# Optimization experiments

Measured on AMD Instinct MI355X. Metric: run time of the kernel, lower is better.

The kernel has to match this reference:

```python
import jax, jax.numpy as jnp
import numpy as np

B, N_SIDE, S = 64, 40, 512
N = N_SIDE * N_SIDE          # 1600 grid points (fl_feature_dims [1,40,40])
EMB = 10                     # embedding_dim
GDIM = 8                     # lie('homography').dim
WIDTH = 128
C1 = 20                      # first-layer output channels


def _embed(x, emb_dim):
    # sinusoidal embedding of each scalar coordinate: [..., D] -> [..., D*emb_dim]
    freqs = 2.0 ** jnp.arange(emb_dim // 2, dtype=x.dtype)
    ang = x[..., None] * freqs                       # [..., D, emb/2]
    e = jnp.concatenate([jnp.sin(ang), jnp.cos(ang)], axis=-1)  # [..., D, emb]
    return e.reshape(x.shape[:-1] + (x.shape[-1] * emb_dim,))


def _glorot(key, shape):
    fan_in = shape[0]
    return jax.random.normal(key, shape, dtype=jnp.float32) / np.sqrt(fan_in)


def setup_inputs() -> dict:
    key = jax.random.key(0)
    ks = jax.random.split(key, 16)
    inp = {
        'data':   jax.random.normal(ks[0], (B, N, 1), dtype=jnp.float32),
        'v0':     jax.random.normal(ks[1], (S, GDIM), dtype=jnp.float32),
        'v_last': jax.random.normal(ks[2], (S, GDIM), dtype=jnp.float32),
        # FirstLayer filter MLP: 2*EMB -> 20 -> 20 -> 1*C1
        'fl_w1': _glorot(ks[3], (2 * EMB, 20)), 'fl_b1': jnp.zeros((20,), jnp.float32),
        'fl_w2': _glorot(ks[4], (20, 20)),      'fl_b2': jnp.zeros((20,), jnp.float32),
        'fl_w3': _glorot(ks[5], (20, C1)),      'fl_b3': jnp.zeros((C1,), jnp.float32),
        # Hidden FilterMLP: EMB*GDIM=80 -> WIDTH -> C1*WIDTH
        's_w1': _glorot(ks[6], (EMB * GDIM, WIDTH)), 's_b1': jnp.zeros((WIDTH,), jnp.float32),
        's_w2': _glorot(ks[7], (WIDTH, C1 * WIDTH)), 's_b2': jnp.zeros((C1 * WIDTH,), jnp.float32),
        'fc1_w': _glorot(ks[8], (WIDTH, WIDTH)), 'fc1_b': jnp.zeros((WIDTH,), jnp.float32),
        'fc2_w': _glorot(ks[9], (WIDTH, WIDTH)), 'fc2_b': jnp.zeros((WIDTH,), jnp.float32),
        'pool_w': _glorot(ks[10], (WIDTH, 10)),  'pool_b': jnp.zeros((10,), jnp.float32),
    }
    return inp


def reference(data, v0, v_last, fl_w1, fl_b1, fl_w2, fl_b2, fl_w3, fl_b3,
              s_w1, s_b1, s_w2, s_b2, fc1_w, fc1_b, fc2_w, fc2_b, pool_w, pool_b):
    silu = jax.nn.silu
    # pixel grid in [-1,1]^2, homogeneous coords [N,3]
    lin = jnp.linspace(-1.0, 1.0, N_SIDE, dtype=data.dtype)
    xx, yy = jnp.meshgrid(lin, lin, indexing='ij')
    coords = jnp.stack([xx.ravel(), yy.ravel()], axis=-1)           # [N,2]
    xh = jnp.concatenate([coords, jnp.ones((N, 1), data.dtype)], -1)  # [N,3]
    # homography matrices: identity + small perturbation from 8 group params
    pert = jnp.concatenate([0.1 * v_last, jnp.zeros((S, 1), data.dtype)], -1).reshape(S, 3, 3)
    H = jnp.eye(3, dtype=data.dtype) + pert                          # [S,3,3]
    y = jnp.einsum('sij,nj->sni', H, xh)                             # [S,N,3]
    t = y[..., :2] / y[..., 2:3]                                     # projective action [S,N,2]
    # continuous-kernel first layer: filters generated by MLP on embedded coords
    e1 = _embed(t, EMB)                                              # [S,N,20]
    h = silu(e1 @ fl_w1 + fl_b1)
    h = silu(h @ fl_w2 + fl_b2)
    filt1 = h @ fl_w3 + fl_b3                                        # [S,N,C1]
    z = jnp.einsum('bn,sno->bso', data[:, :, 0], filt1) / N          # [B,S,C1]
    z = silu(z)
    # hidden FilterMLP on group samples v0 -> per-sample filters [S,C1,WIDTH]
    v0e = _embed(v0, EMB)                                            # [S,80]
    h2 = silu(v0e @ s_w1 + s_b1)                                     # [S,WIDTH]
    filt2 = (h2 @ s_w2 + s_b2).reshape(S, C1, WIDTH)
    # (1/S) * sum over group-sample and channel axes of broadcast product
    z = jnp.einsum('bsc,scw->bw', z, filt2) / S                      # [B,WIDTH]
    z = silu(z @ fc1_w + fc1_b) + z
    z = silu(z @ fc2_w + fc2_b) + z
    return z @ pool_w + pool_b                                       # [B,10]
```

## Files before the change

kernel.cpp:

```cpp
#include <hip/hip_runtime.h>

#define N_PTS 1600
#define NSIDE 40
#define SNUM  512
#define BNUM  64
#define C1D   20
#define WID   128

typedef _Float16 h8  __attribute__((ext_vector_type(8)));
typedef _Float16 h4  __attribute__((ext_vector_type(4)));
typedef __fp16   h2v __attribute__((ext_vector_type(2)));
typedef float    f4  __attribute__((ext_vector_type(4)));

__device__ __forceinline__ float silu_f(float x){ return x / (1.f + __expf(-x)); }
__device__ __forceinline__ void fma4(float4& a, float s, const float4 w){
    a.x += s*w.x; a.y += s*w.y; a.z += s*w.z; a.w += s*w.w;
}

__global__ __launch_bounds__(256) void ka_prep(
    const float* __restrict__ data, const float* __restrict__ v0,
    const float* __restrict__ s_w1, const float* __restrict__ s_b1,
    const float* __restrict__ s_w2, const float* __restrict__ s_b2,
    const float* __restrict__ w1, const float* __restrict__ b1,
    const float* __restrict__ w2, const float* __restrict__ b2,
    const float* __restrict__ w3, const float* __restrict__ b3,
    _Float16* __restrict__ dataA, float* __restrict__ f2g,
    _Float16* __restrict__ wPackA, float* __restrict__ bPackA,
    float* __restrict__ out2g)
{
    const int t  = threadIdx.x;
    const int bx = blockIdx.x;
    if (bx == 370) {
        const float* wsrc[3] = { w1, w2, w3 };
        const float* bsrc[3] = { b1, b2, b3 };
        for (int v = t; v < 3072; v += 256) {
            const int l = v >> 10, rem = v & 1023;
            const int cout = rem >> 5, cin = rem & 31;
            float x = 0.f;
            if (cout < 20 && cin < 20) x = wsrc[l][cin * 20 + cout];
            wPackA[v] = (_Float16)x;
        }
        if (t < 96) {
            const int l = t >> 5, cout = t & 31;
            bPackA[t] = (cout < 20) ? bsrc[l][cout] : 0.f;
        }
        for (int v = t; v < 8192; v += 256) out2g[v] = 0.f;
        return;
    }
    if (bx >= 320) {
        const int o  = (bx - 320) * 256 + t;
        const int L  = o & 63, cm = o >> 6;
        const int mt = cm & 3, ch = cm >> 2;
        const int b  = mt * 16 + (L & 15);
        const int nb = ch * 32 + (L >> 4) * 8;
        const float* src = data + b * N_PTS + nb;
        h8 v;
        #pragma unroll
        for (int j = 0; j < 8; j++) v[j] = (_Float16)src[j];
        *(h8*)(dataA + (size_t)o * 8) = v;
        return;
    }
    const int st  = bx / 10, ct = bx - st * 10;
    const int s0  = st * 16;
    const int col = ct * 256 + t;
    __shared__ __align__(16) float h2t[128][20];

    for (int idx = t; idx < 2048; idx += 256) {
        const int ss = idx >> 7, j = idx & 127;
        float acc = s_b1[j];
        #pragma unroll
        for (int d = 0; d < 8; d++) {
            const float val = v0[(s0 + ss) * 8 + d];
            float sv, cv;
            __sincosf(val, &sv, &cv);
            #pragma unroll
            for (int k = 0; k < 5; k++) {
                acc += sv * s_w1[(d*10 + k)     * WID + j];
                acc += cv * s_w1[(d*10 + 5 + k) * WID + j];
                const float ns = 2.f * sv * cv;
                const float nc = 1.f - 2.f * sv * sv;
                sv = ns; cv = nc;
            }
        }
        h2t[j][ss] = silu_f(acc);
    }
    __syncthreads();

    float4 acc[4];
    #pragma unroll
    for (int qq = 0; qq < 4; qq++) acc[qq] = make_float4(0.f, 0.f, 0.f, 0.f);
    #pragma unroll 4
    for (int i = 0; i < 128; i++) {
        const float wv = s_w2[i * 2560 + col];
        const float4* hh = (const float4*)&h2t[i][0];
        #pragma unroll
        for (int qq = 0; qq < 4; qq++) fma4(acc[qq], wv, hh[qq]);
    }
    const float bias = s_b2[col];
    const float* af = (const float*)acc;
    #pragma unroll
    for (int ss = 0; ss < 16; ss++)
        f2g[(s0 + ss) * 2560 + col] = af[ss] + bias;
}

__device__ __forceinline__ void embed_pt(int n, const float Hm[9], h2v e2[10])
{
    const int i = n / NSIDE;
    const int j = n - i * NSIDE;
    const float x = -1.f + (float)i * (2.f/39.f);
    const float y = -1.f + (float)j * (2.f/39.f);
    const float y0 = Hm[0]*x + Hm[1]*y + Hm[2];
    const float y1 = Hm[3]*x + Hm[4]*y + Hm[5];
    const float y2 = Hm[6]*x + Hm[7]*y + Hm[8];
    const float inv = 1.f / y2;
    const float t0 = y0 * inv, t1 = y1 * inv;
    float e[20];
    float sv0, cv0, sv1, cv1;
    __sincosf(t0, &sv0, &cv0);
    __sincosf(t1, &sv1, &cv1);
    #pragma unroll
    for (int k = 0; k < 5; k++) {
        e[k] = sv0; e[5+k] = cv0; e[10+k] = sv1; e[15+k] = cv1;
        const float ns0 = 2.f*sv0*cv0, nc0 = 1.f - 2.f*sv0*sv0; sv0 = ns0; cv0 = nc0;
        const float ns1 = 2.f*sv1*cv1, nc1 = 1.f - 2.f*sv1*sv1; sv1 = ns1; cv1 = nc1;
    }
    #pragma unroll
    for (int k = 0; k < 10; k++)
        e2[k] = __builtin_amdgcn_cvt_pkrtz(e[2*k], e[2*k+1]);
}

#define ASTRIDE 40

__global__ __launch_bounds__(256) void k1_filt_z(
    const _Float16* __restrict__ dataA, const float* __restrict__ v_last,
    const _Float16* __restrict__ wPackA, const float* __restrict__ bPackA,
    float* __restrict__ zpart)
{
    const int s    = blockIdx.x & 511;
    const int half = blockIdx.x >> 9;
    const int nb0  = half * 800;
    const int t    = threadIdx.x;
    const int lane = t & 63;
    const int w    = t >> 6;
    const int q    = lane >> 4;
    const int l15  = lane & 15;

    __shared__ __align__(16) unsigned char pool[21504];
    __shared__ __align__(16) _Float16 filtB[20 * 264];
    _Float16* act = (_Float16*)pool;
    float*    red = (float*)pool;

    h8 wf[3][2]; float bv[3][2];
    #pragma unroll
    for (int l = 0; l < 3; l++)
        #pragma unroll
        for (int nt = 0; nt < 2; nt++) {
            wf[l][nt] = *(const h8*)(wPackA + (((l*2+nt)*16 + l15) * 32 + q*8));
            bv[l][nt] = bPackA[(l*2+nt)*16 + l15];
        }

    float Hm[9];
    #pragma unroll
    for (int k = 0; k < 9; k++) Hm[k] = (k == 0 || k == 4 || k == 8) ? 1.f : 0.f;
    #pragma unroll
    for (int k = 0; k < 8; k++) Hm[k] += 0.1f * v_last[s*8 + k];

    f4 zacc[4][2];
    #pragma unroll
    for (int mt = 0; mt < 4; mt++) { zacc[mt][0] = (f4)(0.f); zacc[mt][1] = (f4)(0.f); }
    const f4 zero4 = (f4)(0.f);

    {
        unsigned long long* pz = (unsigned long long*)(act + t*ASTRIDE + 20);
        pz[0] = 0ull; pz[1] = 0ull; pz[2] = 0ull;
    }

    for (int base = 0; base < 800; base += 256) {
        const int tn = min(256, 800 - base);
        if (t < tn) {
            h2v e2[10];
            embed_pt(nb0 + base + t, Hm, e2);
            #pragma unroll
            for (int k = 0; k < 10; k++)
                *(h2v*)(act + t*ASTRIDE + 2*k) = e2[k];
        }
        __syncthreads();

        const int nmt = tn >> 4;
        #pragma unroll
        for (int l = 0; l < 3; l++) {
            for (int mt = w; mt < nmt; mt += 4) {
                const int r0 = mt * 16;
                const h8 af = *(const h8*)(act + (r0 + l15)*ASTRIDE + q*8);
                f4 D0 = __builtin_amdgcn_mfma_f32_16x16x32_f16(af, wf[l][0], zero4, 0, 0, 0);
                f4 D1 = __builtin_amdgcn_mfma_f32_16x16x32_f16(af, wf[l][1], zero4, 0, 0, 0);
                if (l < 2) {
                    #pragma unroll
                    for (int r = 0; r < 4; r++) {
                        const int p = r0 + q*4 + r;
                        act[p*ASTRIDE + l15] = (_Float16)silu_f(D0[r] + bv[l][0]);
                        if (l15 < 4)
                            act[p*ASTRIDE + 16 + l15] = (_Float16)silu_f(D1[r] + bv[l][1]);
                    }
                } else {
                    h4 p0, p1;
                    #pragma unroll
                    for (int r = 0; r < 4; r++) {
                        p0[r] = (_Float16)(D0[r] + bv[2][0]);
                        p1[r] = (_Float16)(D1[r] + bv[2][1]);
                    }
                    *(h4*)(filtB + l15*264 + r0 + q*4) = p0;
                    if (l15 < 4)
                        *(h4*)(filtB + (16 + l15)*264 + r0 + q*4) = p1;
                }
            }
        }
        __syncthreads();

        const int nkc = tn >> 5;
        const int r1row = (l15 < 4) ? (16 + l15) : 0;
        for (int kc = w; kc < nkc; kc += 4) {
            const int gchunk = ((nb0 + base) >> 5) + kc;
            const h8 bf0 = *(const h8*)(filtB + l15  *264 + kc*32 + q*8);
            const h8 bf1 = *(const h8*)(filtB + r1row*264 + kc*32 + q*8);
            #pragma unroll
            for (int mt = 0; mt < 4; mt++) {
                const h8 afz = *(const h8*)(dataA + ((size_t)(gchunk*4 + mt)*64 + lane)*8);
                zacc[mt][0] = __builtin_amdgcn_mfma_f32_16x16x32_f16(afz, bf0, zacc[mt][0], 0, 0, 0);
                zacc[mt][1] = __builtin_amdgcn_mfma_f32_16x16x32_f16(afz, bf1, zacc[mt][1], 0, 0, 0);
            }
        }
        __syncthreads();
    }

    #pragma unroll
    for (int mt = 0; mt < 4; mt++) {
        #pragma unroll
        for (int r = 0; r < 4; r++) {
            const int b = mt*16 + q*4 + r;
            red[(w*64 + b)*21 + l15] = zacc[mt][0][r];
            if (l15 < 4) red[(w*64 + b)*21 + 16 + l15] = zacc[mt][1][r];
        }
    }
    __syncthreads();
    for (int v = t; v < 1280; v += 256) {
        const int c = v >> 6, b = v & 63;
        const float sum = red[b*21 + c] + red[(64+b)*21 + c]
                        + red[(128+b)*21 + c] + red[(192+b)*21 + c];
        zpart[(half*512 + s)*1280 + v] = sum;
    }
}

__global__ __launch_bounds__(256) void k2_contract(
    const float* __restrict__ zg, const float* __restrict__ f2g,
    float* __restrict__ out2g)
{
    const int blk = blockIdx.x;
    const int sg  = blk >> 1;
    const int wh  = blk & 1;
    const int s0  = sg * 4;
    const int w0  = wh * 64;
    const int t   = threadIdx.x;
    __shared__ __align__(16) float zl[4*1280];
    __shared__ __align__(16) float fl[4*20*64];
    #pragma unroll
    for (int sp = 0; sp < 4; sp++) {
        const int srow = (s0 + sp) * 1280;
        for (int r = t; r < 1280; r += 256) {
            const float a0 = zg[srow + r];
            const float a1 = zg[512*1280 + srow + r];
            zl[sp*1280 + r] = silu_f((a0 + a1) * (1.f / (float)N_PTS));
        }
        for (int u = t; u < 1280; u += 256) {
            const int c = u >> 6, ww = u & 63;
            fl[sp*1280 + u] = f2g[(s0 + sp)*2560 + c*128 + w0 + ww];
        }
    }
    __syncthreads();
    const int ww = t & 63, bh = t >> 6;
    float4 acc[4];
    #pragma unroll
    for (int qq = 0; qq < 4; qq++) acc[qq] = make_float4(0.f, 0.f, 0.f, 0.f);
    #pragma unroll 4
    for (int sc = 0; sc < 80; sc++) {
        const float f = fl[sc * 64 + ww];
        const float4* zz = (const float4*)&zl[sc * 64 + bh * 16];
        #pragma unroll
        for (int qq = 0; qq < 4; qq++) fma4(acc[qq], f, zz[qq]);
    }
    const float* af = (const float*)acc;
    #pragma unroll
    for (int idx = 0; idx < 16; idx++) {
        const int b = bh * 16 + idx;
        atomicAdd(&out2g[b * 128 + w0 + ww], af[idx]);
    }
}

__global__ __launch_bounds__(128) void k3_tail(
    const float* __restrict__ out2g,
    const float* __restrict__ fc1w, const float* __restrict__ fc1b,
    const float* __restrict__ fc2w, const float* __restrict__ fc2b,
    const float* __restrict__ pw,   const float* __restrict__ pb,
    float* __restrict__ out)
{
    const int b = blockIdx.x, t = threadIdx.x;
    __shared__ float zb[128], r1[128], r2[128];
    zb[t] = out2g[b * 128 + t] * (1.f / (float)SNUM);
    __syncthreads();
    float a = fc1b[t];
    #pragma unroll 8
    for (int i = 0; i < 128; i++) a += zb[i] * fc1w[i * 128 + t];
    r1[t] = silu_f(a) + zb[t];
    __syncthreads();
    a = fc2b[t];
    #pragma unroll 8
    for (int i = 0; i < 128; i++) a += r1[i] * fc2w[i * 128 + t];
    r2[t] = silu_f(a) + r1[t];
    __syncthreads();
    if (t < 10) {
        float o = pb[t];
        #pragma unroll 8
        for (int i = 0; i < 128; i++) o += r2[i] * pw[i * 10 + t];
        out[b * 10 + t] = o;
    }
}

extern "C" void kernel_launch(void* const* d_in, const int* in_sizes, int n_in,
                              void* d_out, int out_size, void* d_ws, size_t ws_size,
                              hipStream_t stream) {
    const float* data   = (const float*)d_in[0];
    const float* v0     = (const float*)d_in[1];
    const float* v_last = (const float*)d_in[2];
    const float* fl_w1  = (const float*)d_in[3];
    const float* fl_b1  = (const float*)d_in[4];
    const float* fl_w2  = (const float*)d_in[5];
    const float* fl_b2  = (const float*)d_in[6];
    const float* fl_w3  = (const float*)d_in[7];
    const float* fl_b3  = (const float*)d_in[8];
    const float* s_w1   = (const float*)d_in[9];
    const float* s_b1   = (const float*)d_in[10];
    const float* s_w2   = (const float*)d_in[11];
    const float* s_b2   = (const float*)d_in[12];
    const float* fc1_w  = (const float*)d_in[13];
    const float* fc1_b  = (const float*)d_in[14];
    const float* fc2_w  = (const float*)d_in[15];
    const float* fc2_b  = (const float*)d_in[16];
    const float* pool_w = (const float*)d_in[17];
    const float* pool_b = (const float*)d_in[18];
    float* out = (float*)d_out;

    float* ws        = (float*)d_ws;
    _Float16* dataA  = (_Float16*)ws;
    float* zpart  = ws    + 51200;
    float* f2g    = zpart + 1310720;
    float* out2g  = f2g   + 1310720;
    _Float16* wPackA = (_Float16*)(out2g + 8192);
    float* bPackA = out2g + 8192 + 1536;

    ka_prep    <<<371, 256, 0, stream>>>(data, v0, s_w1, s_b1, s_w2, s_b2,
                                         fl_w1, fl_b1, fl_w2, fl_b2, fl_w3, fl_b3,
                                         dataA, f2g, wPackA, bPackA, out2g);
    k1_filt_z  <<<1024, 256, 0, stream>>>(dataA, v_last, wPackA, bPackA, zpart);
    k2_contract<<<256, 256, 0, stream>>>(zpart, f2g, out2g);
    k3_tail    <<<64, 128, 0, stream>>>(out2g, fc1_w, fc1_b, fc2_w, fc2_b,
                                        pool_w, pool_b, out);
}
```

Before: 192.6 us.

## Double k1 block size to 512 threads, stage MLP weights in LDS, use fast reciprocals

```diff
diff --git a/kernel.cpp b/kernel.cpp
--- a/kernel.cpp
+++ b/kernel.cpp
@@ -12,7 +12,9 @@
 typedef __fp16   h2v __attribute__((ext_vector_type(2)));
 typedef float    f4  __attribute__((ext_vector_type(4)));
 
-__device__ __forceinline__ float silu_f(float x){ return x / (1.f + __expf(-x)); }
+__device__ __forceinline__ float silu_f(float x){
+    return x * __builtin_amdgcn_rcpf(1.f + __expf(-x));
+}
 __device__ __forceinline__ void fma4(float4& a, float s, const float4 w){
     a.x += s*w.x; a.y += s*w.y; a.z += s*w.z; a.w += s*w.w;
 }
@@ -112,7 +114,7 @@
     const float y0 = Hm[0]*x + Hm[1]*y + Hm[2];
     const float y1 = Hm[3]*x + Hm[4]*y + Hm[5];
     const float y2 = Hm[6]*x + Hm[7]*y + Hm[8];
-    const float inv = 1.f / y2;
+    const float inv = __builtin_amdgcn_rcpf(y2);
     const float t0 = y0 * inv, t1 = y1 * inv;
     float e[20];
     float sv0, cv0, sv1, cv1;
@@ -131,7 +133,7 @@
 
 #define ASTRIDE 40
 
-__global__ __launch_bounds__(256) void k1_filt_z(
+__global__ __launch_bounds__(512, 8) void k1_filt_z(
     const _Float16* __restrict__ dataA, const float* __restrict__ v_last,
     const _Float16* __restrict__ wPackA, const float* __restrict__ bPackA,
     float* __restrict__ zpart)
@@ -144,20 +146,19 @@
     const int w    = t >> 6;
     const int q    = lane >> 4;
     const int l15  = lane & 15;
+    const int mtbase = (w & 1) * 2;
+    const int kcs    = w >> 1;
 
     __shared__ __align__(16) unsigned char pool[21504];
     __shared__ __align__(16) _Float16 filtB[20 * 264];
+    __shared__ __align__(16) _Float16 wlds[3072];
+    __shared__ __align__(16) float    blds[96];
     _Float16* act = (_Float16*)pool;
     float*    red = (float*)pool;
 
-    h8 wf[3][2]; float bv[3][2];
-    #pragma unroll
-    for (int l = 0; l < 3; l++)
-        #pragma unroll
-        for (int nt = 0; nt < 2; nt++) {
-            wf[l][nt] = *(const h8*)(wPackA + (((l*2+nt)*16 + l15) * 32 + q*8));
-            bv[l][nt] = bPackA[(l*2+nt)*16 + l15];
-        }
+    for (int v = t; v < 1536; v += 512)
+        ((unsigned int*)wlds)[v] = ((const unsigned int*)wPackA)[v];
+    if (t < 96) blds[t] = bPackA[t];
 
     float Hm[9];
     #pragma unroll
@@ -165,12 +166,12 @@
     #pragma unroll
     for (int k = 0; k < 8; k++) Hm[k] += 0.1f * v_last[s*8 + k];
 
-    f4 zacc[4][2];
-    #pragma unroll
-    for (int mt = 0; mt < 4; mt++) { zacc[mt][0] = (f4)(0.f); zacc[mt][1] = (f4)(0.f); }
+    f4 zacc[2][2];
+    #pragma unroll
+    for (int mi = 0; mi < 2; mi++) { zacc[mi][0] = (f4)(0.f); zacc[mi][1] = (f4)(0.f); }
     const f4 zero4 = (f4)(0.f);
 
-    {
+    if (t < 256) {
         unsigned long long* pz = (unsigned long long*)(act + t*ASTRIDE + 20);
         pz[0] = 0ull; pz[1] = 0ull; pz[2] = 0ull;
     }
@@ -189,25 +190,29 @@
         const int nmt = tn >> 4;
         #pragma unroll
         for (int l = 0; l < 3; l++) {
-            for (int mt = w; mt < nmt; mt += 4) {
+            const h8 wf0 = *(const h8*)(wlds + ((l*2+0)*16 + l15) * 32 + q*8);
+            const h8 wf1 = *(const h8*)(wlds + ((l*2+1)*16 + l15) * 32 + q*8);
+            const float b0 = blds[(l*2+0)*16 + l15];
+            const float b1 = blds[(l*2+1)*16 + l15];
+            for (int mt = w; mt < nmt; mt += 8) {
                 const int r0 = mt * 16;
                 const h8 af = *(const h8*)(act + (r0 + l15)*ASTRIDE + q*8);
-                f4 D0 = __builtin_amdgcn_mfma_f32_16x16x32_f16(af, wf[l][0], zero4, 0, 0, 0);
-                f4 D1 = __builtin_amdgcn_mfma_f32_16x16x32_f16(af, wf[l][1], zero4, 0, 0, 0);
+                f4 D0 = __builtin_amdgcn_mfma_f32_16x16x32_f16(af, wf0, zero4, 0, 0, 0);
+                f4 D1 = __builtin_amdgcn_mfma_f32_16x16x32_f16(af, wf1, zero4, 0, 0, 0);
                 if (l < 2) {
                     #pragma unroll
                     for (int r = 0; r < 4; r++) {
                         const int p = r0 + q*4 + r;
-                        act[p*ASTRIDE + l15] = (_Float16)silu_f(D0[r] + bv[l][0]);
+                        act[p*ASTRIDE + l15] = (_Float16)silu_f(D0[r] + b0);
                         if (l15 < 4)
-                            act[p*ASTRIDE + 16 + l15] = (_Float16)silu_f(D1[r] + bv[l][1]);
+                            act[p*ASTRIDE + 16 + l15] = (_Float16)silu_f(D1[r] + b1);
                     }
                 } else {
                     h4 p0, p1;
                     #pragma unroll
                     for (int r = 0; r < 4; r++) {
-                        p0[r] = (_Float16)(D0[r] + bv[2][0]);
-                        p1[r] = (_Float16)(D1[r] + bv[2][1]);
+                        p0[r] = (_Float16)(D0[r] + b0);
+                        p1[r] = (_Float16)(D1[r] + b1);
                     }
                     *(h4*)(filtB + l15*264 + r0 + q*4) = p0;
                     if (l15 < 4)
@@ -219,34 +224,42 @@
 
         const int nkc = tn >> 5;
         const int r1row = (l15 < 4) ? (16 + l15) : 0;
-        for (int kc = w; kc < nkc; kc += 4) {
-            const int gchunk = ((nb0 + base) >> 5) + kc;
-            const h8 bf0 = *(const h8*)(filtB + l15  *264 + kc*32 + q*8);
-            const h8 bf1 = *(const h8*)(filtB + r1row*264 + kc*32 + q*8);
-            #pragma unroll
-            for (int mt = 0; mt < 4; mt++) {
-                const h8 afz = *(const h8*)(dataA + ((size_t)(gchunk*4 + mt)*64 + lane)*8);
-                zacc[mt][0] = __builtin_amdgcn_mfma_f32_16x16x32_f16(afz, bf0, zacc[mt][0], 0, 0, 0);
-                zacc[mt][1] = __builtin_amdgcn_mfma_f32_16x16x32_f16(afz, bf1, zacc[mt][1], 0, 0, 0);
+        #pragma unroll
+        for (int kk = 0; kk < 2; kk++) {
+            const int kc = kcs + kk*4;
+            if (kc < nkc) {
+                const int gchunk = ((nb0 + base) >> 5) + kc;
+                const h8 bf0 = *(const h8*)(filtB + l15  *264 + kc*32 + q*8);
+                const h8 bf1 = *(const h8*)(filtB + r1row*264 + kc*32 + q*8);
+                #pragma unroll
+                for (int mi = 0; mi < 2; mi++) {
+                    const int mt = mtbase + mi;
+                    const h8 afz = *(const h8*)(dataA + ((size_t)(gchunk*4 + mt)*64 + lane)*8);
+                    zacc[mi][0] = __builtin_amdgcn_mfma_f32_16x16x32_f16(afz, bf0, zacc[mi][0], 0, 0, 0);
+                    zacc[mi][1] = __builtin_amdgcn_mfma_f32_16x16x32_f16(afz, bf1, zacc[mi][1], 0, 0, 0);
+                }
             }
         }
         __syncthreads();
     }
 
     #pragma unroll
-    for (int mt = 0; mt < 4; mt++) {
+    for (int mi = 0; mi < 2; mi++) {
         #pragma unroll
         for (int r = 0; r < 4; r++) {
-            const int b = mt*16 + q*4 + r;
-            red[(w*64 + b)*21 + l15] = zacc[mt][0][r];
-            if (l15 < 4) red[(w*64 + b)*21 + 16 + l15] = zacc[mt][1][r];
-        }
-    }
-    __syncthreads();
-    for (int v = t; v < 1280; v += 256) {
+            const int bl = mi*16 + q*4 + r;
+            red[(w*32 + bl)*21 + l15] = zacc[mi][0][r];
+            if (l15 < 4) red[(w*32 + bl)*21 + 16 + l15] = zacc[mi][1][r];
+        }
+    }
+    __syncthreads();
+    for (int v = t; v < 1280; v += 512) {
         const int c = v >> 6, b = v & 63;
-        const float sum = red[b*21 + c] + red[(64+b)*21 + c]
-                        + red[(128+b)*21 + c] + red[(192+b)*21 + c];
+        const int mts = b >> 5, bl = b & 31;
+        const float sum = red[((mts    )*32 + bl)*21 + c]
+                        + red[((mts + 2)*32 + bl)*21 + c]
+                        + red[((mts + 4)*32 + bl)*21 + c]
+                        + red[((mts + 6)*32 + bl)*21 + c];
         zpart[(half*512 + s)*1280 + v] = sum;
     }
 }
@@ -360,7 +373,7 @@
     ka_prep    <<<371, 256, 0, stream>>>(data, v0, s_w1, s_b1, s_w2, s_b2,
                                          fl_w1, fl_b1, fl_w2, fl_b2, fl_w3, fl_b3,
                                          dataA, f2g, wPackA, bPackA, out2g);
-    k1_filt_z  <<<1024, 256, 0, stream>>>(dataA, v_last, wPackA, bPackA, zpart);
+    k1_filt_z  <<<1024, 512, 0, stream>>>(dataA, v_last, wPackA, bPackA, zpart);
     k2_contract<<<256, 256, 0, stream>>>(zpart, f2g, out2g);
     k3_tail    <<<64, 128, 0, stream>>>(out2g, fc1_w, fc1_b, fc2_w, fc2_b,
                                         pool_w, pool_b, out);
```

Measured after the change: 181.3 us. -5.8%, faster.
